# Kernel tuning notes

Measured on AMD Instinct MI355X. Metric: run time of the kernel, lower is better.

## Reference

```python
import jax, jax.numpy as jnp
import numpy as np

STATE_DIM, ACTION_DIM, HIDDEN, ACTOR_HIDDEN = 64, 8, 256, 256
B, T = 1024, 512


def _uniform(key, shape, bound):
    return jax.random.uniform(key, shape, jnp.float32, -bound, bound)


def setup_inputs() -> dict:
    key = jax.random.key(0)
    ks = jax.random.split(key, 12)
    k = 1.0 / np.sqrt(HIDDEN)  # PyTorch GRU/Linear init bound
    ka = 1.0 / np.sqrt(ACTOR_HIDDEN)
    return {
        "x_seq": jax.random.normal(ks[0], (B, T, STATE_DIM), jnp.float32),
        # GRU params (PyTorch layout: [3*H, in] with gate order r,z,n)
        "w_ih": _uniform(ks[1], (3 * HIDDEN, STATE_DIM), k),
        "w_hh": _uniform(ks[2], (3 * HIDDEN, HIDDEN), k),
        "b_ih": _uniform(ks[3], (3 * HIDDEN,), k),
        "b_hh": _uniform(ks[4], (3 * HIDDEN,), k),
        # base MLP
        "w_base": _uniform(ks[5], (ACTOR_HIDDEN, HIDDEN), k),
        "b_base": _uniform(ks[6], (ACTOR_HIDDEN,), k),
        # factorized heads
        "w_dir": _uniform(ks[7], (ACTION_DIM, ACTOR_HIDDEN), ka),
        "b_dir": _uniform(ks[8], (ACTION_DIM,), ka),
        "w_mag": _uniform(ks[9], (ACTION_DIM, ACTOR_HIDDEN), ka),
        "b_mag": _uniform(ks[10], (ACTION_DIM,), ka),
    }


def reference(x_seq, w_ih, w_hh, b_ih, b_hh, w_base, b_base, w_dir, b_dir, w_mag, b_mag):
    H = w_hh.shape[1]

    def step(h, x_t):
        gi = x_t @ w_ih.T + b_ih          # [B, 3H]
        gh = h @ w_hh.T + b_hh            # [B, 3H]
        i_r, i_z, i_n = jnp.split(gi, 3, axis=-1)
        h_r, h_z, h_n = jnp.split(gh, 3, axis=-1)
        r = jax.nn.sigmoid(i_r + h_r)
        z = jax.nn.sigmoid(i_z + h_z)
        n = jnp.tanh(i_n + r * h_n)
        h_new = (1.0 - z) * n + z * h
        return h_new, None

    h0 = jnp.zeros((x_seq.shape[0], H), x_seq.dtype)
    last, _ = jax.lax.scan(step, h0, jnp.swapaxes(x_seq, 0, 1))  # carry = h_T
    h = jax.nn.relu(last @ w_base.T + b_base)
    direction = jnp.tanh(h @ w_dir.T + b_dir)
    magnitude = jax.nn.sigmoid(h @ w_mag.T + b_mag)
    return direction * magnitude
```

## Files before the change

kernel.cpp:

```cpp
#include <hip/hip_runtime.h>

#define T_SEQ 512
#define HID 256

typedef _Float16 half8 __attribute__((ext_vector_type(8)));
typedef _Float16 half4 __attribute__((ext_vector_type(4)));
typedef float floatx4 __attribute__((ext_vector_type(4)));

#define OFF_GH 0
#define OFF_GI (OFF_GH + 384 * 512)
#define OFF_WB (OFF_GI + 96 * 512)
#define OFF_WD (OFF_WB + 128 * 512)

#define GI_OFF_BYTES (4ull << 20)
#define GI_T_STRIDE 3072ull
#define GI_B_STRIDE (512ull * 3072ull)
#define WS_NEED (GI_OFF_BYTES + 64ull * GI_B_STRIDE * 8ull)

#define MFMA16(A, B, C) __builtin_amdgcn_mfma_f32_16x16x32_f16(A, B, C, 0, 0, 0)

__device__ __forceinline__ float sigm(float x) { return 1.0f / (1.0f + __expf(-x)); }
__device__ __forceinline__ float tanh_fast(float x) {
  float e = __expf(2.0f * x);
  return 1.0f - 2.0f / (e + 1.0f);
}

__global__ void prep_kernel(const float* __restrict__ w_ih,
                            const float* __restrict__ w_hh,
                            const float* __restrict__ w_base,
                            const float* __restrict__ w_dir,
                            const float* __restrict__ w_mag,
                            _Float16* __restrict__ ws) {
  const int f = blockIdx.x;
  const int lane = threadIdx.x;
  const int col = lane & 15, quad = lane >> 4;
  const float* src;
  int n, k, ld;
  _Float16* dst;
  if (f < 384) {
    int nt = f % 6, kt = (f / 6) % 8, w = f / 48;
    n = (nt >> 1) * 256 + w * 32 + (nt & 1) * 16 + col;
    k = kt * 32 + quad * 8;
    src = w_hh; ld = 256;
    dst = ws + OFF_GH + ((w * 8 + kt) * 6 + nt) * 512 + lane * 8;
  } else if (f < 480) {
    int f2 = f - 384;
    int nt = f2 % 6, kt = (f2 / 6) % 2, w = f2 / 12;
    n = (nt >> 1) * 256 + w * 32 + (nt & 1) * 16 + col;
    k = kt * 32 + quad * 8;
    src = w_ih; ld = 64;
    dst = ws + OFF_GI + ((w * 2 + kt) * 6 + nt) * 512 + lane * 8;
  } else if (f < 608) {
    int f3 = f - 480;
    int nt = f3 % 2, kt = (f3 / 2) % 8, w = f3 / 16;
    n = w * 32 + nt * 16 + col;
    k = kt * 32 + quad * 8;
    src = w_base; ld = 256;
    dst = ws + OFF_WB + ((w * 8 + kt) * 2 + nt) * 512 + lane * 8;
  } else {
    int kt = f - 608;
    k = kt * 32 + quad * 8;
    ld = 256;
    if (col < 8) { src = w_dir; n = col; } else { src = w_mag; n = col - 8; }
    dst = ws + OFF_WD + kt * 512 + lane * 8;
  }
#pragma unroll
  for (int j = 0; j < 8; ++j)
    dst[j] = (_Float16)src[n * ld + k + j];
}

__global__ __launch_bounds__(512, 1)
void gi_prepass_kernel(const float* __restrict__ x_seq,
                       const float* __restrict__ b_ih,
                       const float* __restrict__ b_hh,
                       const _Float16* __restrict__ ws,
                       uint2* __restrict__ gi_out) {
  const int tid = threadIdx.x;
  const int lane = tid & 63;
  const int w = tid >> 6;
  const int col = lane & 15;
  const int quad = lane >> 4;
  const int btile = blockIdx.x >> 2, tq = blockIdx.x & 3;
  const int row0 = btile * 16;

  const half8* __restrict__ gip = (const half8*)(ws + OFF_GI) + w * (12 * 64);
  half8 wg[12];
#pragma unroll
  for (int f = 0; f < 12; ++f) wg[f] = gip[f * 64 + lane];

  float bias[6];
#pragma unroll
  for (int a = 0; a < 6; ++a) {
    const int c = w * 32 + (a & 1) * 16 + col;
    const int g = a >> 1;
    bias[a] = (g < 2) ? (b_ih[g * 256 + c] + b_hh[g * 256 + c]) : b_ih[512 + c];
  }

  const float* const xlane = x_seq + (size_t)(row0 + col) * (T_SEQ * 64) + quad * 8;
  uint2* const gout = gi_out + (size_t)btile * GI_B_STRIDE + (size_t)w * 384 + lane;

  float4 xc[4], xn[4];
  {
    const float* p = xlane + (size_t)(tq * 128) * 64;
    xc[0] = *(const float4*)(p);
    xc[1] = *(const float4*)(p + 4);
    xc[2] = *(const float4*)(p + 32);
    xc[3] = *(const float4*)(p + 36);
  }

#pragma unroll 1
  for (int tt = 0; tt < 128; ++tt) {
    const int t = tq * 128 + tt;
    if (tt + 1 < 128) {
      const float* p = xlane + (size_t)(t + 1) * 64;
      xn[0] = *(const float4*)(p);
      xn[1] = *(const float4*)(p + 4);
      xn[2] = *(const float4*)(p + 32);
      xn[3] = *(const float4*)(p + 36);
    }
    half8 ax0, ax1;
#pragma unroll
    for (int j = 0; j < 4; ++j) {
      ax0[j]     = (_Float16)((const float*)&xc[0])[j];
      ax0[4 + j] = (_Float16)((const float*)&xc[1])[j];
      ax1[j]     = (_Float16)((const float*)&xc[2])[j];
      ax1[4 + j] = (_Float16)((const float*)&xc[3])[j];
    }

    floatx4 acc[6];
#pragma unroll
    for (int a = 0; a < 6; ++a) acc[a] = (floatx4){0.f, 0.f, 0.f, 0.f};
#pragma unroll
    for (int nt = 0; nt < 6; ++nt) {
      acc[nt] = MFMA16(ax0, wg[nt], acc[nt]);
      acc[nt] = MFMA16(ax1, wg[6 + nt], acc[nt]);
    }

    uint2* gp = gout + (size_t)t * GI_T_STRIDE;
#pragma unroll
    for (int a = 0; a < 6; ++a) {
      union { uint2 u; half4 h; } pk;
#pragma unroll
      for (int r2 = 0; r2 < 4; ++r2)
        pk.h[r2] = (_Float16)(acc[a][r2] + bias[a]);
      gp[a * 64] = pk.u;
    }
#pragma unroll
    for (int i = 0; i < 4; ++i) xc[i] = xn[i];
  }
}

__global__ __launch_bounds__(512, 2)
void gru_main_kernel(const float* __restrict__ b_hh,
                     const float* __restrict__ b_base,
                     const float* __restrict__ b_dir,
                     const float* __restrict__ b_mag,
                     const _Float16* __restrict__ ws,
                     const uint2* __restrict__ gi_in,
                     float* __restrict__ out) {
  __shared__ __align__(16) _Float16 hlin[2][4096];

  const int tid = threadIdx.x;
  const int lane = tid & 63;
  const int w = tid >> 6;
  const int col = lane & 15;
  const int quad = lane >> 4;
  const int row0 = blockIdx.x * 16;

  *(half8*)&hlin[0][tid * 8] = (half8)((_Float16)0.0f);

  float bhn[2];
#pragma unroll
  for (int s = 0; s < 2; ++s) bhn[s] = b_hh[512 + w * 32 + s * 16 + col];

  float hreg[2][4];
#pragma unroll
  for (int s = 0; s < 2; ++s)
#pragma unroll
    for (int r2 = 0; r2 < 4; ++r2) hreg[s][r2] = 0.0f;

  const half8* __restrict__ ghp = (const half8*)(ws + OFF_GH) + w * (48 * 64);
  const half8* __restrict__ wbp = (const half8*)(ws + OFF_WB) + w * (16 * 64);
  const half8* __restrict__ wdp = (const half8*)(ws + OFF_WD);

  half8 wreg[16];
#pragma unroll
  for (int f = 0; f < 16; ++f) wreg[f] = ghp[f * 64 + lane];

  const uint2* const gilane =
      gi_in + (size_t)blockIdx.x * GI_B_STRIDE + (size_t)w * 384 + lane;

#pragma unroll 1
  for (int t = 0; t < T_SEQ; ++t) {
    __syncthreads();
    const int cur = t & 1;
    const _Float16* hc = hlin[cur];
    _Float16* hn = hlin[cur ^ 1];

    uint2 g[6];
    const uint2* gp = gilane + (size_t)t * GI_T_STRIDE;
#pragma unroll
    for (int a = 0; a < 6; ++a) g[a] = gp[a * 64];

    half8 s1[8], s2[8];
#pragma unroll
    for (int i = 0; i < 8; ++i) s1[i] = ghp[(16 + i) * 64 + lane];
#pragma unroll
    for (int i = 0; i < 8; ++i) s2[i] = ghp[(24 + i) * 64 + lane];

    half8 ah[8];
#pragma unroll
    for (int kt = 0; kt < 8; ++kt)
      ah[kt] = *(const half8*)&hc[kt * 512 + lane * 8];

    floatx4 acc[6];
#pragma unroll
    for (int a = 0; a < 6; ++a) acc[a] = (floatx4){0.f, 0.f, 0.f, 0.f};

#pragma unroll
    for (int f = 0; f < 16; ++f)
      acc[f % 6] = MFMA16(ah[f / 6], wreg[f], acc[f % 6]);

    half8 s3[8];
#pragma unroll
    for (int i = 0; i < 8; ++i) s3[i] = ghp[(32 + i) * 64 + lane];

#pragma unroll
    for (int i = 0; i < 8; ++i) {
      const int f = 16 + i;
      acc[f % 6] = MFMA16(ah[f / 6], s1[i], acc[f % 6]);
    }

    half8 s4[8];
#pragma unroll
    for (int i = 0; i < 8; ++i) s4[i] = ghp[(40 + i) * 64 + lane];

#pragma unroll
    for (int i = 0; i < 8; ++i) {
      const int f = 24 + i;
      acc[f % 6] = MFMA16(ah[f / 6], s2[i], acc[f % 6]);
    }
#pragma unroll
    for (int i = 0; i < 8; ++i) {
      const int f = 32 + i;
      acc[f % 6] = MFMA16(ah[f / 6], s3[i], acc[f % 6]);
    }
#pragma unroll
    for (int i = 0; i < 8; ++i) {
      const int f = 40 + i;
      acc[f % 6] = MFMA16(ah[f / 6], s4[i], acc[f % 6]);
    }

#pragma unroll
    for (int s = 0; s < 2; ++s) {
      const int inner = s * 16 + col;
      const int widx = w * 512 + (inner >> 3) * 128 + (col & 7);
      union { uint2 u; half4 h; } gr, gz, gn;
      gr.u = g[0 + s]; gz.u = g[2 + s]; gn.u = g[4 + s];
#pragma unroll
      for (int r2 = 0; r2 < 4; ++r2) {
        const float rr = sigm(acc[0 + s][r2] + (float)gr.h[r2]);
        const float zz = sigm(acc[2 + s][r2] + (float)gz.h[r2]);
        const float nn = tanh_fast((float)gn.h[r2] + rr * (acc[4 + s][r2] + bhn[s]));
        const float hnew = zz * hreg[s][r2] + (1.0f - zz) * nn;
        hreg[s][r2] = hnew;
        hn[widx + (quad * 4 + r2) * 8] = (_Float16)hnew;
      }
    }
  }

  __syncthreads();
  {
    floatx4 ab[2];
    ab[0] = (floatx4){0.f, 0.f, 0.f, 0.f};
    ab[1] = (floatx4){0.f, 0.f, 0.f, 0.f};
#pragma unroll
    for (int kt = 0; kt < 8; ++kt) {
      const half8 ahh = *(const half8*)&hlin[0][kt * 512 + lane * 8];
      const half8* bp = wbp + kt * (2 * 64) + lane;
      ab[0] = MFMA16(ahh, bp[0],  ab[0]);
      ab[1] = MFMA16(ahh, bp[64], ab[1]);
    }
#pragma unroll
    for (int s = 0; s < 2; ++s) {
      const int inner = s * 16 + col;
      const int widx = w * 512 + (inner >> 3) * 128 + (col & 7);
      const float bb = b_base[w * 32 + inner];
#pragma unroll
      for (int r2 = 0; r2 < 4; ++r2) {
        const float v = ab[s][r2] + bb;
        hlin[1][widx + (quad * 4 + r2) * 8] = (_Float16)fmaxf(v, 0.0f);
      }
    }
  }
  __syncthreads();

  if (w == 0) {
    floatx4 ad = (floatx4){0.f, 0.f, 0.f, 0.f};
#pragma unroll
    for (int kt = 0; kt < 8; ++kt) {
      const half8 ahh = *(const half8*)&hlin[1][kt * 512 + lane * 8];
      ad = MFMA16(ahh, wdp[kt * 64 + lane], ad);
    }
    const float bd = (col < 8) ? b_dir[col] : b_mag[col - 8];
#pragma unroll
    for (int r2 = 0; r2 < 4; ++r2) {
      const float v = ad[r2] + bd;
      const float act = (col < 8) ? tanh_fast(v) : sigm(v);
      const float other = __shfl_xor(act, 8, 64);
      if (col < 8)
        out[(size_t)(row0 + quad * 4 + r2) * 8 + col] = act * other;
    }
  }
}

__global__ __launch_bounds__(512, 2)
void gru_head_fallback(const float* __restrict__ x_seq,
                       const float* __restrict__ b_ih,
                       const float* __restrict__ b_hh,
                       const float* __restrict__ b_base,
                       const float* __restrict__ b_dir,
                       const float* __restrict__ b_mag,
                       const _Float16* __restrict__ ws,
                       float* __restrict__ out) {
  __shared__ __align__(16) _Float16 hlin[2][4096];
  __shared__ __align__(16) _Float16 wlds[8][4096];

  const int tid = threadIdx.x;
  const int lane = tid & 63;
  const int w = tid >> 6;
  const int col = lane & 15;
  const int quad = lane >> 4;
  const int row0 = blockIdx.x * 16;

  *(half8*)&hlin[0][tid * 8] = (half8)((_Float16)0.0f);

  float br[2], bz[2], bin_[2], bhn[2];
#pragma unroll
  for (int s = 0; s < 2; ++s) {
    const int c = w * 32 + s * 16 + col;
    br[s] = b_ih[c] + b_hh[c];
    bz[s] = b_ih[256 + c] + b_hh[256 + c];
    bin_[s] = b_ih[512 + c];
    bhn[s] = b_hh[512 + c];
  }
  float hreg[2][4];
#pragma unroll
  for (int s = 0; s < 2; ++s)
#pragma unroll
    for (int r2 = 0; r2 < 4; ++r2) hreg[s][r2] = 0.0f;

  const half8* __restrict__ ghp = (const half8*)(ws + OFF_GH) + w * (48 * 64);
  const half8* __restrict__ gip = (const half8*)(ws + OFF_GI) + w * (12 * 64);
  const half8* __restrict__ wbp = (const half8*)(ws + OFF_WB) + w * (16 * 64);
  const half8* __restrict__ wdp = (const half8*)(ws + OFF_WD);

  half8 wreg[16];
#pragma unroll
  for (int f = 0; f < 16; ++f) wreg[f] = ghp[f * 64 + lane];
  _Float16* const wlw = wlds[w];
#pragma unroll
  for (int j = 0; j < 8; ++j)
    *(half8*)&wlw[j * 512 + lane * 8] = ghp[(16 + j) * 64 + lane];

  const float* const xlane = x_seq + ((size_t)(row0 + col) * T_SEQ) * 64 + quad * 8;
  float4 xc[4], xn[4];
  {
    const float* p = xlane;
    xc[0] = *(const float4*)(p);
    xc[1] = *(const float4*)(p + 4);
    xc[2] = *(const float4*)(p + 32);
    xc[3] = *(const float4*)(p + 36);
  }

  auto body = [&](int t, int tpre, int cur, float4* xcur, float4* xnext) {
    const int nxt = cur ^ 1;
    __syncthreads();
    half8 s1[6], s2[6];
#pragma unroll
    for (int i = 0; i < 6; ++i) s1[i] = ghp[(24 + i) * 64 + lane];
#pragma unroll
    for (int i = 0; i < 6; ++i) s2[i] = ghp[(30 + i) * 64 + lane];
    {
      const float* p = xlane + (size_t)tpre * 64;
      xnext[0] = *(const float4*)(p);
      xnext[1] = *(const float4*)(p + 4);
      xnext[2] = *(const float4*)(p + 32);
      xnext[3] = *(const float4*)(p + 36);
    }
    half8 ah[8];
#pragma unroll
    for (int kt = 0; kt < 8; ++kt)
      ah[kt] = *(const half8*)&hlin[cur][kt * 512 + lane * 8];
    half8 wl[8];
#pragma unroll
    for (int j = 0; j < 8; ++j)
      wl[j] = *(const half8*)&wlw[j * 512 + lane * 8];
    half8 ax0, ax1;
#pragma unroll
    for (int j = 0; j < 4; ++j) {
      ax0[j]     = (_Float16)((const float*)&xcur[0])[j];
      ax0[4 + j] = (_Float16)((const float*)&xcur[1])[j];
      ax1[j]     = (_Float16)((const float*)&xcur[2])[j];
      ax1[4 + j] = (_Float16)((const float*)&xcur[3])[j];
    }
    floatx4 acc[8];
#pragma unroll
    for (int i = 0; i < 8; ++i) acc[i] = (floatx4){0.f, 0.f, 0.f, 0.f};
#pragma unroll
    for (int f = 0; f < 16; ++f)
      acc[f % 6] = MFMA16(ah[f / 6], wreg[f], acc[f % 6]);
    half8 s3[6];
#pragma unroll
    for (int i = 0; i < 6; ++i) s3[i] = ghp[(36 + i) * 64 + lane];
#pragma unroll
    for (int j = 0; j < 8; ++j) {
      const int f = 16 + j;
      acc[f % 6] = MFMA16(ah[f / 6], wl[j], acc[f % 6]);
    }
#pragma unroll
    for (int i = 0; i < 6; ++i) {
      const int f = 24 + i;
      acc[f % 6] = MFMA16(ah[f / 6], s1[i], acc[f % 6]);
    }
    half8 s4[6];
#pragma unroll
    for (int i = 0; i < 6; ++i) s4[i] = ghp[(42 + i) * 64 + lane];
#pragma unroll
    for (int i = 0; i < 6; ++i) {
      const int f = 30 + i;
      acc[f % 6] = MFMA16(ah[f / 6], s2[i], acc[f % 6]);
    }
    half8 s5[6];
#pragma unroll
    for (int i = 0; i < 6; ++i) s5[i] = gip[i * 64 + lane];
#pragma unroll
    for (int i = 0; i < 6; ++i) {
      const int f = 36 + i;
      acc[f % 6] = MFMA16(ah[f / 6], s3[i], acc[f % 6]);
    }
    half8 s6[6];
#pragma unroll
    for (int i = 0; i < 6; ++i) s6[i] = gip[(6 + i) * 64 + lane];
#pragma unroll
    for (int i = 0; i < 6; ++i) {
      const int f = 42 + i;
      acc[f % 6] = MFMA16(ah[f / 6], s4[i], acc[f % 6]);
    }
#pragma unroll
    for (int i = 0; i < 6; ++i) {
      const int aidx = (i < 4) ? i : i + 2;
      acc[aidx] = MFMA16(ax0, s5[i], acc[aidx]);
    }
#pragma unroll
    for (int i = 0; i < 6; ++i) {
      const int aidx = (i < 4) ? i : i + 2;
      acc[aidx] = MFMA16(ax1, s6[i], acc[aidx]);
    }
#pragma unroll
    for (int s = 0; s < 2; ++s) {
      const int inner = s * 16 + col;
      const int widx = w * 512 + (inner >> 3) * 128 + (col & 7);
#pragma unroll
      for (int r2 = 0; r2 < 4; ++r2) {
        const float rr = sigm(acc[0 + s][r2] + br[s]);
        const float zz = sigm(acc[2 + s][r2] + bz[s]);
        const float nn = tanh_fast(acc[6 + s][r2] + bin_[s] + rr * (acc[4 + s][r2] + bhn[s]));
        const float hnew = zz * hreg[s][r2] + (1.0f - zz) * nn;
        hreg[s][r2] = hnew;
        hlin[nxt][widx + (quad * 4 + r2) * 8] = (_Float16)hnew;
      }
    }
  };

#pragma unroll 1
  for (int t = 0; t < T_SEQ; t += 2) {
    body(t, t + 1, 0, xc, xn);
    const int tp2 = (t + 2 < T_SEQ) ? (t + 2) : (T_SEQ - 1);
    body(t + 1, tp2, 1, xn, xc);
  }

  __syncthreads();
  {
    floatx4 ab[2];
    ab[0] = (floatx4){0.f, 0.f, 0.f, 0.f};
    ab[1] = (floatx4){0.f, 0.f, 0.f, 0.f};
#pragma unroll
    for (int kt = 0; kt < 8; ++kt) {
      const half8 ahh = *(const half8*)&hlin[0][kt * 512 + lane * 8];
      const half8* bp = wbp + kt * (2 * 64) + lane;
      ab[0] = MFMA16(ahh, bp[0],  ab[0]);
      ab[1] = MFMA16(ahh, bp[64], ab[1]);
    }
#pragma unroll
    for (int s = 0; s < 2; ++s) {
      const int inner = s * 16 + col;
      const int widx = w * 512 + (inner >> 3) * 128 + (col & 7);
      const float bb = b_base[w * 32 + inner];
#pragma unroll
      for (int r2 = 0; r2 < 4; ++r2) {
        const float v = ab[s][r2] + bb;
        hlin[1][widx + (quad * 4 + r2) * 8] = (_Float16)fmaxf(v, 0.0f);
      }
    }
  }
  __syncthreads();
  if (w == 0) {
    floatx4 ad = (floatx4){0.f, 0.f, 0.f, 0.f};
#pragma unroll
    for (int kt = 0; kt < 8; ++kt) {
      const half8 ahh = *(const half8*)&hlin[1][kt * 512 + lane * 8];
      ad = MFMA16(ahh, wdp[kt * 64 + lane], ad);
    }
    const float bd = (col < 8) ? b_dir[col] : b_mag[col - 8];
#pragma unroll
    for (int r2 = 0; r2 < 4; ++r2) {
      const float v = ad[r2] + bd;
      const float act = (col < 8) ? tanh_fast(v) : sigm(v);
      const float other = __shfl_xor(act, 8, 64);
      if (col < 8)
        out[(size_t)(row0 + quad * 4 + r2) * 8 + col] = act * other;
    }
  }
}

extern "C" void kernel_launch(void* const* d_in, const int* in_sizes, int n_in,
                              void* d_out, int out_size, void* d_ws, size_t ws_size,
                              hipStream_t stream) {
  const float* x_seq  = (const float*)d_in[0];
  const float* b_ih   = (const float*)d_in[3];
  const float* b_hh   = (const float*)d_in[4];
  const float* b_base = (const float*)d_in[6];
  const float* b_dir  = (const float*)d_in[8];
  const float* b_mag  = (const float*)d_in[10];
  _Float16* ws = (_Float16*)d_ws;
  float* out = (float*)d_out;

  hipLaunchKernelGGL(prep_kernel, dim3(616), dim3(64), 0, stream,
                     (const float*)d_in[1], (const float*)d_in[2],
                     (const float*)d_in[5], (const float*)d_in[7],
                     (const float*)d_in[9], ws);

  if (ws_size >= WS_NEED) {
    uint2* gi = (uint2*)((char*)d_ws + GI_OFF_BYTES);
    hipLaunchKernelGGL(gi_prepass_kernel, dim3(256), dim3(512), 0, stream,
                       x_seq, b_ih, b_hh, ws, gi);
    hipLaunchKernelGGL(gru_main_kernel, dim3(64), dim3(512), 0, stream,
                       b_hh, b_base, b_dir, b_mag, ws, gi, out);
  } else {
    hipLaunchKernelGGL(gru_head_fallback, dim3(64), dim3(512), 0, stream,
                       x_seq, b_ih, b_hh, b_base, b_dir, b_mag, ws, out);
  }
}
```

Baseline: 2.197 ms.

## Chunk time dimension across prepass/recurrence launches and keep more W_hh in registers

Instead of precomputing input-gate activations for the full sequence into a large workspace buffer, the timeline is split into chunks of 128, 64 or 32 steps, whichever fits the workspace. Each chunk gets a prepass launch followed by a recurrent launch that saves and restores the hidden state through a global buffer. The recurrent kernel also drops to one block per CU and keeps 40 of its 48 W_hh fragments resident in registers, instead of streaming most of them each step. This shrinks the gi buffer so it can stay cache-resident and cuts per-step weight loads, at the cost of extra launches, serialized prepass phases and higher register pressure.

```diff
diff --git a/kernel.cpp b/kernel.cpp
--- a/kernel.cpp
+++ b/kernel.cpp
@@ -11,11 +11,8 @@
 #define OFF_GI (OFF_GH + 384 * 512)
 #define OFF_WB (OFF_GI + 96 * 512)
 #define OFF_WD (OFF_WB + 128 * 512)
-
-#define GI_OFF_BYTES (4ull << 20)
-#define GI_T_STRIDE 3072ull
-#define GI_B_STRIDE (512ull * 3072ull)
-#define WS_NEED (GI_OFF_BYTES + 64ull * GI_B_STRIDE * 8ull)
+#define HSAVE_OFF_BYTES (4ull << 20)
+#define GI_OFF_BYTES (6ull << 20)
 
 #define MFMA16(A, B, C) __builtin_amdgcn_mfma_f32_16x16x32_f16(A, B, C, 0, 0, 0)
 
@@ -74,14 +71,16 @@
                        const float* __restrict__ b_ih,
                        const float* __restrict__ b_hh,
                        const _Float16* __restrict__ ws,
-                       uint2* __restrict__ gi_out) {
+                       uint2* __restrict__ gi_out,
+                       int t0, int nTq, int chunk) {
   const int tid = threadIdx.x;
   const int lane = tid & 63;
   const int w = tid >> 6;
   const int col = lane & 15;
   const int quad = lane >> 4;
-  const int btile = blockIdx.x >> 2, tq = blockIdx.x & 3;
+  const int btile = blockIdx.x / nTq, tq = blockIdx.x % nTq;
   const int row0 = btile * 16;
+  const int tstart = t0 + tq * 32;
 
   const half8* __restrict__ gip = (const half8*)(ws + OFF_GI) + w * (12 * 64);
   half8 wg[12];
@@ -97,11 +96,12 @@
   }
 
   const float* const xlane = x_seq + (size_t)(row0 + col) * (T_SEQ * 64) + quad * 8;
-  uint2* const gout = gi_out + (size_t)btile * GI_B_STRIDE + (size_t)w * 384 + lane;
+  uint2* const gout = gi_out + (size_t)btile * ((size_t)chunk * 3072) +
+                      (size_t)w * 384 + lane;
 
   float4 xc[4], xn[4];
   {
-    const float* p = xlane + (size_t)(tq * 128) * 64;
+    const float* p = xlane + (size_t)tstart * 64;
     xc[0] = *(const float4*)(p);
     xc[1] = *(const float4*)(p + 4);
     xc[2] = *(const float4*)(p + 32);
@@ -109,9 +109,9 @@
   }
 
 #pragma unroll 1
-  for (int tt = 0; tt < 128; ++tt) {
-    const int t = tq * 128 + tt;
-    if (tt + 1 < 128) {
+  for (int tt = 0; tt < 32; ++tt) {
+    const int t = tstart + tt;
+    if (tt + 1 < 32) {
       const float* p = xlane + (size_t)(t + 1) * 64;
       xn[0] = *(const float4*)(p);
       xn[1] = *(const float4*)(p + 4);
@@ -136,7 +136,7 @@
       acc[nt] = MFMA16(ax1, wg[6 + nt], acc[nt]);
     }
 
-    uint2* gp = gout + (size_t)t * GI_T_STRIDE;
+    uint2* gp = gout + (size_t)(t - t0) * 3072;
 #pragma unroll
     for (int a = 0; a < 6; ++a) {
       union { uint2 u; half4 h; } pk;
@@ -150,14 +150,16 @@
   }
 }
 
-__global__ __launch_bounds__(512, 2)
+__global__ __launch_bounds__(512, 1)
 void gru_main_kernel(const float* __restrict__ b_hh,
                      const float* __restrict__ b_base,
                      const float* __restrict__ b_dir,
                      const float* __restrict__ b_mag,
                      const _Float16* __restrict__ ws,
                      const uint2* __restrict__ gi_in,
-                     float* __restrict__ out) {
+                     float* __restrict__ hsave,
+                     float* __restrict__ out,
+                     int chunk, int first, int last) {
   __shared__ __align__(16) _Float16 hlin[2][4096];
 
   const int tid = threadIdx.x;
@@ -167,46 +169,57 @@
   const int quad = lane >> 4;
   const int row0 = blockIdx.x * 16;
 
-  *(half8*)&hlin[0][tid * 8] = (half8)((_Float16)0.0f);
-
   float bhn[2];
 #pragma unroll
   for (int s = 0; s < 2; ++s) bhn[s] = b_hh[512 + w * 32 + s * 16 + col];
 
   float hreg[2][4];
-#pragma unroll
-  for (int s = 0; s < 2; ++s)
-#pragma unroll
-    for (int r2 = 0; r2 < 4; ++r2) hreg[s][r2] = 0.0f;
+  if (first) {
+#pragma unroll
+    for (int s = 0; s < 2; ++s)
+#pragma unroll
+      for (int r2 = 0; r2 < 4; ++r2) hreg[s][r2] = 0.0f;
+    *(half8*)&hlin[0][tid * 8] = (half8)((_Float16)0.0f);
+  } else {
+    const float* hp = hsave + ((size_t)blockIdx.x * 512 + tid) * 8;
+#pragma unroll
+    for (int s = 0; s < 2; ++s) {
+      const int inner = s * 16 + col;
+      const int widx = w * 512 + (inner >> 3) * 128 + (col & 7);
+#pragma unroll
+      for (int r2 = 0; r2 < 4; ++r2) {
+        hreg[s][r2] = hp[s * 4 + r2];
+        hlin[0][widx + (quad * 4 + r2) * 8] = (_Float16)hreg[s][r2];
+      }
+    }
+  }
 
   const half8* __restrict__ ghp = (const half8*)(ws + OFF_GH) + w * (48 * 64);
   const half8* __restrict__ wbp = (const half8*)(ws + OFF_WB) + w * (16 * 64);
   const half8* __restrict__ wdp = (const half8*)(ws + OFF_WD);
 
-  half8 wreg[16];
-#pragma unroll
-  for (int f = 0; f < 16; ++f) wreg[f] = ghp[f * 64 + lane];
+  half8 wreg[40];
+#pragma unroll
+  for (int f = 0; f < 40; ++f) wreg[f] = ghp[f * 64 + lane];
 
   const uint2* const gilane =
-      gi_in + (size_t)blockIdx.x * GI_B_STRIDE + (size_t)w * 384 + lane;
+      gi_in + (size_t)blockIdx.x * ((size_t)chunk * 3072) + (size_t)w * 384 + lane;
 
 #pragma unroll 1
-  for (int t = 0; t < T_SEQ; ++t) {
+  for (int tl = 0; tl < chunk; ++tl) {
     __syncthreads();
-    const int cur = t & 1;
+    const int cur = tl & 1;
     const _Float16* hc = hlin[cur];
     _Float16* hn = hlin[cur ^ 1];
 
     uint2 g[6];
-    const uint2* gp = gilane + (size_t)t * GI_T_STRIDE;
+    const uint2* gp = gilane + (size_t)tl * 3072;
 #pragma unroll
     for (int a = 0; a < 6; ++a) g[a] = gp[a * 64];
 
-    half8 s1[8], s2[8];
-#pragma unroll
-    for (int i = 0; i < 8; ++i) s1[i] = ghp[(16 + i) * 64 + lane];
-#pragma unroll
-    for (int i = 0; i < 8; ++i) s2[i] = ghp[(24 + i) * 64 + lane];
+    half8 st[8];
+#pragma unroll
+    for (int i = 0; i < 8; ++i) st[i] = ghp[(40 + i) * 64 + lane];
 
     half8 ah[8];
 #pragma unroll
@@ -218,37 +231,12 @@
     for (int a = 0; a < 6; ++a) acc[a] = (floatx4){0.f, 0.f, 0.f, 0.f};
 
 #pragma unroll
-    for (int f = 0; f < 16; ++f)
+    for (int f = 0; f < 40; ++f)
       acc[f % 6] = MFMA16(ah[f / 6], wreg[f], acc[f % 6]);
-
-    half8 s3[8];
-#pragma unroll
-    for (int i = 0; i < 8; ++i) s3[i] = ghp[(32 + i) * 64 + lane];
-
-#pragma unroll
-    for (int i = 0; i < 8; ++i) {
-      const int f = 16 + i;
-      acc[f % 6] = MFMA16(ah[f / 6], s1[i], acc[f % 6]);
-    }
-
-    half8 s4[8];
-#pragma unroll
-    for (int i = 0; i < 8; ++i) s4[i] = ghp[(40 + i) * 64 + lane];
-
-#pragma unroll
-    for (int i = 0; i < 8; ++i) {
-      const int f = 24 + i;
-      acc[f % 6] = MFMA16(ah[f / 6], s2[i], acc[f % 6]);
-    }
-#pragma unroll
-    for (int i = 0; i < 8; ++i) {
-      const int f = 32 + i;
-      acc[f % 6] = MFMA16(ah[f / 6], s3[i], acc[f % 6]);
-    }
 #pragma unroll
     for (int i = 0; i < 8; ++i) {
       const int f = 40 + i;
-      acc[f % 6] = MFMA16(ah[f / 6], s4[i], acc[f % 6]);
+      acc[f % 6] = MFMA16(ah[f / 6], st[i], acc[f % 6]);
     }
 
 #pragma unroll
@@ -267,6 +255,15 @@
         hn[widx + (quad * 4 + r2) * 8] = (_Float16)hnew;
       }
     }
+  }
+
+  if (!last) {
+    float* hp = hsave + ((size_t)blockIdx.x * 512 + tid) * 8;
+#pragma unroll
+    for (int s = 0; s < 2; ++s)
+#pragma unroll
+      for (int r2 = 0; r2 < 4; ++r2) hp[s * 4 + r2] = hreg[s][r2];
+    return;
   }
 
   __syncthreads();
@@ -541,12 +538,25 @@
                      (const float*)d_in[5], (const float*)d_in[7],
                      (const float*)d_in[9], ws);
 
-  if (ws_size >= WS_NEED) {
+  int chunk = 0;
+  const int cand[3] = {128, 64, 32};
+  for (int i = 0; i < 3; ++i) {
+    const size_t need = GI_OFF_BYTES + 64ull * (size_t)cand[i] * 3072ull * 8ull;
+    if (ws_size >= need) { chunk = cand[i]; break; }
+  }
+
+  if (chunk) {
     uint2* gi = (uint2*)((char*)d_ws + GI_OFF_BYTES);
-    hipLaunchKernelGGL(gi_prepass_kernel, dim3(256), dim3(512), 0, stream,
-                       x_seq, b_ih, b_hh, ws, gi);
-    hipLaunchKernelGGL(gru_main_kernel, dim3(64), dim3(512), 0, stream,
-                       b_hh, b_base, b_dir, b_mag, ws, gi, out);
+    float* hsave = (float*)((char*)d_ws + HSAVE_OFF_BYTES);
+    const int nchunks = T_SEQ / chunk;
+    const int nTq = chunk / 32;
+    for (int c = 0; c < nchunks; ++c) {
+      hipLaunchKernelGGL(gi_prepass_kernel, dim3(64 * nTq), dim3(512), 0, stream,
+                         x_seq, b_ih, b_hh, ws, gi, c * chunk, nTq, chunk);
+      hipLaunchKernelGGL(gru_main_kernel, dim3(64), dim3(512), 0, stream,
+                         b_hh, b_base, b_dir, b_mag, ws, gi, hsave, out,
+                         chunk, (c == 0) ? 1 : 0, (c == nchunks - 1) ? 1 : 0);
+    }
   } else {
     hipLaunchKernelGGL(gru_head_fallback, dim3(64), dim3(512), 0, stream,
                        x_seq, b_ih, b_hh, b_base, b_dir, b_mag, ws, out);
```

After: 1.915 ms. 1.15x faster.
